# Optimization experiments

Measured on AMD Instinct MI355X. Metric: run time of the kernel, lower is better.

## Reference

```python
import jax, jax.numpy as jnp
import numpy as np

N = 4096      # batch (e.g. nodes)
MUL = 128     # multiplicity of every irrep chunk
INV_SQRT3 = 1.0 / float(np.sqrt(3.0))  # CG norm for 1x1->0 and 0x1->1 / 1x0->1
INV_SQRT6 = 1.0 / float(np.sqrt(6.0))  # CG norm for 1x1->1 (Levi-Civita / sqrt(6))

# Levi-Civita tensor eps[i,j,k]
_EPS = np.zeros((3, 3, 3), dtype=np.float32)
for a, b, c in [(0, 1, 2), (1, 2, 0), (2, 0, 1)]:
    _EPS[a, b, c] = 1.0
    _EPS[a, c, b] = -1.0
EPS = jnp.asarray(_EPS)


def setup_inputs() -> dict:
    key = jax.random.key(0)
    ks = jax.random.split(key, 9)
    # e3nn path normalization folded into weight init std:
    # std = 1/sqrt(mul1*mul2*num_paths_into_that_output_irrep)
    std2 = 1.0 / float(np.sqrt(MUL * MUL * 2))  # scalar out: 2 paths
    std3 = 1.0 / float(np.sqrt(MUL * MUL * 3))  # vector out: 3 paths
    W = (MUL, MUL, MUL)
    return {
        "x1_s": jax.random.normal(ks[0], (N, MUL), dtype=jnp.float32),
        "x1_v": jax.random.normal(ks[1], (N, MUL, 3), dtype=jnp.float32),
        "x2_s": jax.random.normal(ks[2], (N, MUL), dtype=jnp.float32),
        "x2_v": jax.random.normal(ks[3], (N, MUL, 3), dtype=jnp.float32),
        "w_sss": jax.random.normal(ks[4], W, dtype=jnp.float32) * std2,
        "w_vvs": jax.random.normal(ks[5], W, dtype=jnp.float32) * std2,
        "w_svv": jax.random.normal(ks[6], W, dtype=jnp.float32) * std3,
        "w_vsv": jax.random.normal(ks[7], W, dtype=jnp.float32) * std3,
        "w_vvv": jax.random.normal(ks[8], W, dtype=jnp.float32) * std3,
    }


def reference(x1_s, x1_v, x2_s, x2_v, w_sss, w_vvs, w_svv, w_vsv, w_vvv):
    # ---- paths into 0e (scalar) output ----
    # 0e x 0e -> 0e : CG = 1
    a = jnp.einsum('nu,uvw->nvw', x1_s, w_sss)           # [N,MUL,MUL]
    out_s = jnp.einsum('nvw,nv->nw', a, x2_s)            # [N,MUL]
    # 1o x 1o -> 0e : CG = delta_ij / sqrt(3)
    dot = jnp.einsum('nui,nvi->nuv', x1_v, x2_v) * INV_SQRT3
    out_s = out_s + jnp.einsum('nuv,uvw->nw', dot, w_vvs)
    # ---- paths into 1o (vector) output ----
    # 0e x 1o -> 1o : CG = delta / sqrt(3)
    b = jnp.einsum('nu,uvw->nvw', x1_s, w_svv)
    out_v = jnp.einsum('nvw,nvk->nwk', b, x2_v) * INV_SQRT3   # [N,MUL,3]
    # 1o x 0e -> 1o : CG = delta / sqrt(3)
    c = jnp.einsum('nv,uvw->nuw', x2_s, w_vsv)
    out_v = out_v + jnp.einsum('nuw,nuk->nwk', c, x1_v) * INV_SQRT3
    # 1o x 1o -> 1o : CG = eps_ijk / sqrt(6)  (cross product)
    c1 = jnp.einsum('nvj,ijk->nvik', x2_v, EPS)               # [N,MUL,3,3]
    cross = jnp.einsum('nui,nvik->nuvk', x1_v, c1)            # [N,MUL,MUL,3]
    out_v = out_v + jnp.einsum('nuvk,uvw->nwk', cross, w_vvv) * INV_SQRT6
    # pack IrrepsArray 128x0e+128x1o as flat [N, 128 + 384]
    return jnp.concatenate([out_s, out_v.reshape(out_v.shape[0], -1)], axis=-1)
```

## Files before the change

### kernel.cpp

```cpp
#include <hip/hip_runtime.h>
#include <hip/hip_bf16.h>


typedef _Float16 f16;
typedef _Float16 f16x8 __attribute__((ext_vector_type(8)));
typedef float f32x4 __attribute__((ext_vector_type(4)));
typedef unsigned u32;

#define WT_BYTES  (5u*4u*128u*4096u*2u)
#define X1_BYTES  (32u*4u*16384u*2u)
#define SLICE_EL  655360u
#define CHUNK_EL  5120u

__device__ __forceinline__ u32 pkmul16(u32 a, u32 b){
    u32 r; asm("v_pk_mul_f16 %0, %1, %2" : "=v"(r) : "v"(a), "v"(b)); return r;
}
__device__ __forceinline__ u32 pkfma16(u32 a, u32 b, u32 c){
    u32 r; asm("v_pk_fma_f16 %0, %1, %2, %3" : "=v"(r) : "v"(a), "v"(b), "v"(c)); return r;
}
__device__ __forceinline__ u32 pkfma16n(u32 a, u32 b, u32 c){
    u32 r; asm("v_pk_fma_f16 %0, %1, %2, %3 neg_lo:[1,0,0] neg_hi:[1,0,0]"
               : "=v"(r) : "v"(a), "v"(b), "v"(c)); return r;
}

union Frag { u32 u[4]; f16x8 v; };
__device__ __forceinline__ f16x8 FR(const u32 a[4]){
    Frag f; f.u[0]=a[0]; f.u[1]=a[1]; f.u[2]=a[2]; f.u[3]=a[3]; return f.v;
}

__device__ __forceinline__ void gl_lds16(const f16* g, f16* l) {
    __builtin_amdgcn_global_load_lds(
        (const __attribute__((address_space(1))) void*)g,
        (__attribute__((address_space(3))) void*)l,
        16, 0, 0);
}

__global__ __launch_bounds__(256) void pack_w_kernel(
    const float* __restrict__ w0, const float* __restrict__ w1,
    const float* __restrict__ w2, const float* __restrict__ w3,
    const float* __restrict__ w4, f16* __restrict__ wt)
{
    __shared__ float tl[64][130];
    const int b = blockIdx.x;
    const int p = b >> 7;
    const int u = b & 127;
    const int usec = u >> 5;
    const int uin  = u & 31;
    const float* src = (p==0)?w0:(p==1)?w1:(p==2)?w2:(p==3)?w3:w4;
    const float scale = (p==0)?1.0f:(p==4)?0.40824829046386302f:0.57735026918962576f;

    for (int h = 0; h < 2; ++h) {
        const float* spR = src + (size_t)u*16384 + (size_t)h*8192;
        #pragma unroll
        for (int k = 0; k < 8; ++k) {
            const int e4 = (k*256 + threadIdx.x) * 4;
            const float4 v4 = *(const float4*)(spR + e4);
            const int vi = e4 >> 7, w = e4 & 127;
            tl[vi][w+0]=v4.x; tl[vi][w+1]=v4.y; tl[vi][w+2]=v4.z; tl[vi][w+3]=v4.w;
        }
        __syncthreads();
        #pragma unroll
        for (int k = 0; k < 4; ++k) {
            const int cid = k*256 + threadIdx.x;
            const int vbh  = cid >> 9;
            const int wsec = (cid >> 7) & 3;
            const int w    = (cid >> 2) & 31;
            const int q    = cid & 3;
            const int vb   = h*2 + vbh;
            const int c    = vb*32 + uin;
            const int qs   = q ^ ((w >> 1) & 3);
            f16x8 t8;
            #pragma unroll
            for (int j = 0; j < 8; ++j)
                t8[j] = (f16)(tl[vbh*32 + q*8 + j][wsec*32 + w] * scale);
            *(f16x8*)(wt + (size_t)(usec*4 + wsec)*SLICE_EL + (size_t)c*CHUNK_EL
                          + p*1024 + w*32 + qs*8) = t8;
        }
        __syncthreads();
    }
}

__global__ __launch_bounds__(256) void pack_x_kernel(
    const float* __restrict__ x1s, const float* __restrict__ x1v,
    const float* __restrict__ x2s, const float* __restrict__ x2v,
    f16* __restrict__ x1g, f16* __restrict__ x2g)
{
    if (blockIdx.x < 128) {
        __shared__ uint2 tl[128][33];
        const int nb = blockIdx.x;
        #pragma unroll
        for (int k = 0; k < 16; ++k) {
            const int idx = k*256 + threadIdx.x;
            const int u = idx & 127, nd = idx >> 7;
            const size_t i = (size_t)(nb*32 + nd)*128 + u;
            union { f16 h[4]; uint2 u2; } tp;
            tp.h[0] = (f16)x1s[i];
            tp.h[1] = (f16)x1v[i*3 + 0];
            tp.h[2] = (f16)x1v[i*3 + 1];
            tp.h[3] = (f16)x1v[i*3 + 2];
            tl[u][nd] = tp.u2;
        }
        __syncthreads();
        uint2* og = (uint2*)x1g;
        const int t = nb >> 2, nd0 = (nb & 3) * 32;
        #pragma unroll
        for (int k = 0; k < 16; ++k) {
            const int idx = k*256 + threadIdx.x;
            const int u = idx >> 5, nd = idx & 31;
            og[(((t*4 + (u>>5))*32 + (u&31)) << 7) + nd0 + nd] = tl[u][nd];
        }
    } else {
        const int tt = (blockIdx.x - 128)*256 + threadIdx.x;
        const int n = tt >> 7, v = tt & 127;
        const size_t b = (size_t)n*512;
        const size_t i = (size_t)n*128 + v;
        x2g[b +   0 + v] = (f16)x2s[i];
        x2g[b + 128 + v] = (f16)x2v[i*3 + 0];
        x2g[b + 256 + v] = (f16)x2v[i*3 + 1];
        x2g[b + 384 + v] = (f16)x2v[i*3 + 2];
    }
}

__global__ __launch_bounds__(512, 4) void tp_main(
    const f16* __restrict__ wt, const f16* __restrict__ x1g,
    const f16* __restrict__ x2g, float* __restrict__ out)
{
    __shared__ __align__(16) f16 wlds[4*CHUNK_EL];
    __shared__ __align__(16) f16 x1lds[16384];

    const int tid  = threadIdx.x;
    const int lane = tid & 63;
    const int wv   = tid >> 6;
    const int kg   = lane >> 4;
    const int lr   = lane & 15;

    const int b    = blockIdx.x;
    const int s    = (b & 7)*2 + ((b >> 3) & 1);
    const int t    = b >> 4;
    const int usec = s >> 2;
    const int wsec = s & 3;

    const f16* wstream = wt + (size_t)s * SLICE_EL;

    int boff[2];
    #pragma unroll
    for (int ct = 0; ct < 2; ++ct) {
        const int wp = ct*16 + lr;
        boff[ct] = wp*32 + ((kg ^ ((wp >> 1) & 3)) * 8);
    }

    {
        const f16* src = x1g + ((size_t)(t*4 + usec) << 14);
        #pragma unroll
        for (int r = 0; r < 4; ++r)
            gl_lds16(src + (wv*4 + r)*512 + lane*8, x1lds + (wv*4 + r)*512);
    }
    if (wv < 5) {
        #pragma unroll
        for (int k = 0; k < 2; ++k) {
            const f16* sc = wstream + k*CHUNK_EL + wv*1024 + lane*8;
            f16* dc = wlds + k*CHUNK_EL + wv*1024;
            gl_lds16(sc, dc);
            gl_lds16(sc + 512, dc + 512);
        }
    }
    __syncthreads();

    f32x4 acc[2][4];
    #pragma unroll
    for (int c2 = 0; c2 < 2; ++c2)
        #pragma unroll
        for (int d = 0; d < 4; ++d)
            acc[c2][d] = (f32x4){0.f, 0.f, 0.f, 0.f};

    u32 xq[4][4];
    const f16* wsrc = wstream + 2*CHUNK_EL + wv*1024 + lane*8;
    const f16* x2base = x2g + ((size_t)(t*128 + wv*16 + lr) << 9) + kg*8;

    for (int vb = 0; vb < 4; ++vb) {
        {
            const f16* xb = x2base + vb*32;
            #pragma unroll
            for (int q = 0; q < 4; ++q) {
                const uint4 h = *(const uint4*)(xb + (q << 7));
                xq[q][0] = h.x; xq[q][1] = h.y; xq[q][2] = h.z; xq[q][3] = h.w;
            }
        }
        for (int u2b = 0; u2b < 32; u2b += 4) {
            #pragma unroll
            for (int uu = 0; uu < 4; ++uu) {
                const int u2 = u2b + uu;
                const int c  = vb*32 + u2;

                if (c < 126 && wv < 5) {
                    f16* dc = wlds + ((uu + 2) & 3)*CHUNK_EL + wv*1024;
                    gl_lds16(wsrc, dc);
                    gl_lds16(wsrc + 512, dc + 512);
                }
                wsrc += CHUNK_EL;

                if (c < 126)       { asm volatile("s_waitcnt vmcnt(4)" ::: "memory"); }
                else if (c == 126) { asm volatile("s_waitcnt vmcnt(2)" ::: "memory"); }
                else               { asm volatile("s_waitcnt vmcnt(0)" ::: "memory"); }
                __builtin_amdgcn_s_barrier();
                __builtin_amdgcn_sched_barrier(0);

                f16x8 bfr[5][2];
                const f16* wb = wlds + uu*CHUNK_EL;
                #pragma unroll
                for (int p = 0; p < 5; ++p)
                    #pragma unroll
                    for (int ct = 0; ct < 2; ++ct)
                        bfr[p][ct] = *(const f16x8*)(wb + p*1024 + boff[ct]);

                const uint2 h1 = *(const uint2*)(x1lds + u2*512 + (wv*16 + lr)*4);
                const u32 ps1 = __builtin_amdgcn_perm(h1.x, h1.x, 0x01000100u);
                u32 pv[3];
                pv[0] = __builtin_amdgcn_perm(h1.x, h1.x, 0x03020302u);
                pv[1] = __builtin_amdgcn_perm(h1.y, h1.y, 0x01000100u);
                pv[2] = __builtin_amdgcn_perm(h1.y, h1.y, 0x03020302u);

                {
                    u32 f0[4], f1[4];
                    #pragma unroll
                    for (int j = 0; j < 4; ++j) {
                        f0[j] = pkmul16(ps1, xq[0][j]);
                        u32 d = pkmul16(pv[0], xq[1][j]);
                        d     = pkfma16(pv[1], xq[2][j], d);
                        f1[j] = pkfma16(pv[2], xq[3][j], d);
                    }
                    #pragma unroll
                    for (int ct = 0; ct < 2; ++ct) {
                        acc[ct][0] = __builtin_amdgcn_mfma_f32_16x16x32_f16(FR(f0), bfr[0][ct], acc[ct][0], 0,0,0);
                        acc[ct][0] = __builtin_amdgcn_mfma_f32_16x16x32_f16(FR(f1), bfr[1][ct], acc[ct][0], 0,0,0);
                    }
                }
                #pragma unroll
                for (int k = 0; k < 3; ++k) {
                    const int k1 = (k+1) % 3, k2 = (k+2) % 3;
                    u32 fa[4], fb[4], fc[4];
                    #pragma unroll
                    for (int j = 0; j < 4; ++j) {
                        fa[j] = pkmul16(ps1,    xq[1+k][j]);
                        fb[j] = pkmul16(pv[k],  xq[0][j]);
                        u32 tx = pkmul16(pv[k1], xq[1+k2][j]);
                        fc[j] = pkfma16n(pv[k2], xq[1+k1][j], tx);
                    }
                    #pragma unroll
                    for (int ct = 0; ct < 2; ++ct) {
                        acc[ct][1+k] = __builtin_amdgcn_mfma_f32_16x16x32_f16(FR(fa), bfr[2][ct], acc[ct][1+k], 0,0,0);
                        acc[ct][1+k] = __builtin_amdgcn_mfma_f32_16x16x32_f16(FR(fb), bfr[3][ct], acc[ct][1+k], 0,0,0);
                        acc[ct][1+k] = __builtin_amdgcn_mfma_f32_16x16x32_f16(FR(fc), bfr[4][ct], acc[ct][1+k], 0,0,0);
                    }
                }
            }
        }
    }

    #pragma unroll
    for (int ct = 0; ct < 2; ++ct) {
        const int w = wsec*32 + ct*16 + lr;
        #pragma unroll
        for (int j = 0; j < 4; ++j) {
            const int n = t*128 + wv*16 + kg*4 + j;
            float* op = out + (size_t)n*512;
            unsafeAtomicAdd(op + w,             acc[ct][0][j]);
            unsafeAtomicAdd(op + 128 + w*3 + 0, acc[ct][1][j]);
            unsafeAtomicAdd(op + 128 + w*3 + 1, acc[ct][2][j]);
            unsafeAtomicAdd(op + 128 + w*3 + 2, acc[ct][3][j]);
        }
    }
}

extern "C" void kernel_launch(void* const* d_in, const int* in_sizes, int n_in,
                              void* d_out, int out_size, void* d_ws, size_t ws_size,
                              hipStream_t stream)
{
    const float* x1s = (const float*)d_in[0];
    const float* x1v = (const float*)d_in[1];
    const float* x2s = (const float*)d_in[2];
    const float* x2v = (const float*)d_in[3];
    const float* w0  = (const float*)d_in[4];
    const float* w1  = (const float*)d_in[5];
    const float* w2  = (const float*)d_in[6];
    const float* w3  = (const float*)d_in[7];
    const float* w4  = (const float*)d_in[8];

    f16* wtb = (f16*)d_ws;
    f16* x1g = (f16*)((char*)d_ws + WT_BYTES);
    f16* x2g = (f16*)((char*)d_ws + WT_BYTES + X1_BYTES);
    float* out = (float*)d_out;

    pack_w_kernel<<<640, 256, 0, stream>>>(w0, w1, w2, w3, w4, wtb);
    pack_x_kernel<<<2176, 256, 0, stream>>>(x1s, x1v, x2s, x2v, x1g, x2g);
    hipMemsetAsync(d_out, 0, (size_t)out_size*sizeof(float), stream);
    tp_main<<<512, 512, 0, stream>>>(wtb, x1g, x2g, out);
}
```

Before: 239.5 us.

## Halve block size, give each wave two row tiles to reuse weight fragments

```diff
diff --git a/kernel.cpp b/kernel.cpp
--- a/kernel.cpp
+++ b/kernel.cpp
@@ -4,6 +4,7 @@
 
 typedef _Float16 f16;
 typedef _Float16 f16x8 __attribute__((ext_vector_type(8)));
+typedef _Float16 h2 __attribute__((ext_vector_type(2)));
 typedef float f32x4 __attribute__((ext_vector_type(4)));
 typedef unsigned u32;
 
@@ -12,21 +13,9 @@
 #define SLICE_EL  655360u
 #define CHUNK_EL  5120u
 
-__device__ __forceinline__ u32 pkmul16(u32 a, u32 b){
-    u32 r; asm("v_pk_mul_f16 %0, %1, %2" : "=v"(r) : "v"(a), "v"(b)); return r;
-}
-__device__ __forceinline__ u32 pkfma16(u32 a, u32 b, u32 c){
-    u32 r; asm("v_pk_fma_f16 %0, %1, %2, %3" : "=v"(r) : "v"(a), "v"(b), "v"(c)); return r;
-}
-__device__ __forceinline__ u32 pkfma16n(u32 a, u32 b, u32 c){
-    u32 r; asm("v_pk_fma_f16 %0, %1, %2, %3 neg_lo:[1,0,0] neg_hi:[1,0,0]"
-               : "=v"(r) : "v"(a), "v"(b), "v"(c)); return r;
-}
-
-union Frag { u32 u[4]; f16x8 v; };
-__device__ __forceinline__ f16x8 FR(const u32 a[4]){
-    Frag f; f.u[0]=a[0]; f.u[1]=a[1]; f.u[2]=a[2]; f.u[3]=a[3]; return f.v;
-}
+__device__ __forceinline__ h2 bc(u32 x){ union{u32 u; h2 h;} c; c.u=x; return c.h; }
+
+union F8 { h2 h[4]; f16x8 v; };
 
 __device__ __forceinline__ void gl_lds16(const f16* g, f16* l) {
     __builtin_amdgcn_global_load_lds(
@@ -121,7 +110,7 @@
     }
 }
 
-__global__ __launch_bounds__(512, 4) void tp_main(
+__global__ __launch_bounds__(256, 2) void tp_main(
     const f16* __restrict__ wt, const f16* __restrict__ x1g,
     const f16* __restrict__ x2g, float* __restrict__ out)
 {
@@ -152,38 +141,41 @@
     {
         const f16* src = x1g + ((size_t)(t*4 + usec) << 14);
         #pragma unroll
-        for (int r = 0; r < 4; ++r)
-            gl_lds16(src + (wv*4 + r)*512 + lane*8, x1lds + (wv*4 + r)*512);
-    }
-    if (wv < 5) {
-        #pragma unroll
-        for (int k = 0; k < 2; ++k) {
-            const f16* sc = wstream + k*CHUNK_EL + wv*1024 + lane*8;
-            f16* dc = wlds + k*CHUNK_EL + wv*1024;
-            gl_lds16(sc, dc);
-            gl_lds16(sc + 512, dc + 512);
-        }
+        for (int r = 0; r < 8; ++r)
+            gl_lds16(src + r*2048 + tid*8, x1lds + r*2048 + wv*512 + lane*8);
+    }
+    #pragma unroll
+    for (int k = 0; k < 2; ++k) {
+        const f16* sc = wstream + k*CHUNK_EL + wv*1280 + lane*8;
+        f16* dc = wlds + k*CHUNK_EL + wv*1280;
+        gl_lds16(sc, dc);
+        gl_lds16(sc + 512, dc + 512);
+        if (lane < 32) gl_lds16(sc + 1024, dc + 1024);
     }
     __syncthreads();
 
-    f32x4 acc[2][4];
-    #pragma unroll
-    for (int c2 = 0; c2 < 2; ++c2)
-        #pragma unroll
-        for (int d = 0; d < 4; ++d)
-            acc[c2][d] = (f32x4){0.f, 0.f, 0.f, 0.f};
-
-    u32 xq[4][4];
-    const f16* wsrc = wstream + 2*CHUNK_EL + wv*1024 + lane*8;
-    const f16* x2base = x2g + ((size_t)(t*128 + wv*16 + lr) << 9) + kg*8;
+    f32x4 acc[2][2][4];
+    #pragma unroll
+    for (int rt = 0; rt < 2; ++rt)
+        #pragma unroll
+        for (int c2 = 0; c2 < 2; ++c2)
+            #pragma unroll
+            for (int d = 0; d < 4; ++d)
+                acc[rt][c2][d] = (f32x4){0.f, 0.f, 0.f, 0.f};
+
+    h2 xq[2][4][4];
+    const f16* wsrc = wstream + 2*CHUNK_EL + wv*1280 + lane*8;
 
     for (int vb = 0; vb < 4; ++vb) {
-        {
-            const f16* xb = x2base + vb*32;
+        #pragma unroll
+        for (int rt = 0; rt < 2; ++rt) {
+            const int n = t*128 + wv*32 + rt*16 + lr;
+            const f16* xb = x2g + ((size_t)n << 9) + kg*8 + vb*32;
             #pragma unroll
             for (int q = 0; q < 4; ++q) {
                 const uint4 h = *(const uint4*)(xb + (q << 7));
-                xq[q][0] = h.x; xq[q][1] = h.y; xq[q][2] = h.z; xq[q][3] = h.w;
+                xq[rt][q][0] = bc(h.x); xq[rt][q][1] = bc(h.y);
+                xq[rt][q][2] = bc(h.z); xq[rt][q][3] = bc(h.w);
             }
         }
         for (int u2b = 0; u2b < 32; u2b += 4) {
@@ -192,16 +184,17 @@
                 const int u2 = u2b + uu;
                 const int c  = vb*32 + u2;
 
-                if (c < 126 && wv < 5) {
-                    f16* dc = wlds + ((uu + 2) & 3)*CHUNK_EL + wv*1024;
+                if (c < 126) {
+                    f16* dc = wlds + ((uu + 2) & 3)*CHUNK_EL + wv*1280;
                     gl_lds16(wsrc, dc);
                     gl_lds16(wsrc + 512, dc + 512);
+                    if (lane < 32) gl_lds16(wsrc + 1024, dc + 1024);
                 }
                 wsrc += CHUNK_EL;
 
-                if (c < 126)       { asm volatile("s_waitcnt vmcnt(4)" ::: "memory"); }
-                else if (c == 126) { asm volatile("s_waitcnt vmcnt(2)" ::: "memory"); }
-                else               { asm volatile("s_waitcnt vmcnt(0)" ::: "memory"); }
+                if (u2 == 0 || c == 126) { asm volatile("s_waitcnt vmcnt(3)" ::: "memory"); }
+                else if (c == 127)       { asm volatile("s_waitcnt vmcnt(0)" ::: "memory"); }
+                else                     { asm volatile("s_waitcnt vmcnt(6)" ::: "memory"); }
                 __builtin_amdgcn_s_barrier();
                 __builtin_amdgcn_sched_barrier(0);
 
@@ -213,44 +206,47 @@
                     for (int ct = 0; ct < 2; ++ct)
                         bfr[p][ct] = *(const f16x8*)(wb + p*1024 + boff[ct]);
 
-                const uint2 h1 = *(const uint2*)(x1lds + u2*512 + (wv*16 + lr)*4);
-                const u32 ps1 = __builtin_amdgcn_perm(h1.x, h1.x, 0x01000100u);
-                u32 pv[3];
-                pv[0] = __builtin_amdgcn_perm(h1.x, h1.x, 0x03020302u);
-                pv[1] = __builtin_amdgcn_perm(h1.y, h1.y, 0x01000100u);
-                pv[2] = __builtin_amdgcn_perm(h1.y, h1.y, 0x03020302u);
-
-                {
-                    u32 f0[4], f1[4];
-                    #pragma unroll
-                    for (int j = 0; j < 4; ++j) {
-                        f0[j] = pkmul16(ps1, xq[0][j]);
-                        u32 d = pkmul16(pv[0], xq[1][j]);
-                        d     = pkfma16(pv[1], xq[2][j], d);
-                        f1[j] = pkfma16(pv[2], xq[3][j], d);
+                #pragma unroll
+                for (int rt = 0; rt < 2; ++rt) {
+                    const uint2 h1 = *(const uint2*)(x1lds + u2*512 + (wv*32 + rt*16 + lr)*4);
+                    const h2 ps1 = bc(__builtin_amdgcn_perm(h1.x, h1.x, 0x01000100u));
+                    h2 pv[3];
+                    pv[0] = bc(__builtin_amdgcn_perm(h1.x, h1.x, 0x03020302u));
+                    pv[1] = bc(__builtin_amdgcn_perm(h1.y, h1.y, 0x01000100u));
+                    pv[2] = bc(__builtin_amdgcn_perm(h1.y, h1.y, 0x03020302u));
+
+                    {
+                        F8 f0, f1;
+                        #pragma unroll
+                        for (int j = 0; j < 4; ++j) {
+                            f0.h[j] = ps1 * xq[rt][0][j];
+                            h2 d = pv[0] * xq[rt][1][j];
+                            d = __builtin_elementwise_fma(pv[1], xq[rt][2][j], d);
+                            f1.h[j] = __builtin_elementwise_fma(pv[2], xq[rt][3][j], d);
+                        }
+                        #pragma unroll
+                        for (int ct = 0; ct < 2; ++ct) {
+                            acc[rt][ct][0] = __builtin_amdgcn_mfma_f32_16x16x32_f16(f0.v, bfr[0][ct], acc[rt][ct][0], 0,0,0);
+                            acc[rt][ct][0] = __builtin_amdgcn_mfma_f32_16x16x32_f16(f1.v, bfr[1][ct], acc[rt][ct][0], 0,0,0);
+                        }
                     }
                     #pragma unroll
-                    for (int ct = 0; ct < 2; ++ct) {
-                        acc[ct][0] = __builtin_amdgcn_mfma_f32_16x16x32_f16(FR(f0), bfr[0][ct], acc[ct][0], 0,0,0);
-                        acc[ct][0] = __builtin_amdgcn_mfma_f32_16x16x32_f16(FR(f1), bfr[1][ct], acc[ct][0], 0,0,0);
-                    }
-                }
-                #pragma unroll
-                for (int k = 0; k < 3; ++k) {
-                    const int k1 = (k+1) % 3, k2 = (k+2) % 3;
-                    u32 fa[4], fb[4], fc[4];
-                    #pragma unroll
-                    for (int j = 0; j < 4; ++j) {
-                        fa[j] = pkmul16(ps1,    xq[1+k][j]);
-                        fb[j] = pkmul16(pv[k],  xq[0][j]);
-                        u32 tx = pkmul16(pv[k1], xq[1+k2][j]);
-                        fc[j] = pkfma16n(pv[k2], xq[1+k1][j], tx);
-                    }
-                    #pragma unroll
-                    for (int ct = 0; ct < 2; ++ct) {
-                        acc[ct][1+k] = __builtin_amdgcn_mfma_f32_16x16x32_f16(FR(fa), bfr[2][ct], acc[ct][1+k], 0,0,0);
-                        acc[ct][1+k] = __builtin_amdgcn_mfma_f32_16x16x32_f16(FR(fb), bfr[3][ct], acc[ct][1+k], 0,0,0);
-                        acc[ct][1+k] = __builtin_amdgcn_mfma_f32_16x16x32_f16(FR(fc), bfr[4][ct], acc[ct][1+k], 0,0,0);
+                    for (int k = 0; k < 3; ++k) {
+                        const int k1 = (k+1) % 3, k2 = (k+2) % 3;
+                        F8 fa, fb, fc;
+                        #pragma unroll
+                        for (int j = 0; j < 4; ++j) {
+                            fa.h[j] = ps1   * xq[rt][1+k][j];
+                            fb.h[j] = pv[k] * xq[rt][0][j];
+                            h2 tx = pv[k1] * xq[rt][1+k2][j];
+                            fc.h[j] = __builtin_elementwise_fma(-pv[k2], xq[rt][1+k1][j], tx);
+                        }
+                        #pragma unroll
+                        for (int ct = 0; ct < 2; ++ct) {
+                            acc[rt][ct][1+k] = __builtin_amdgcn_mfma_f32_16x16x32_f16(fa.v, bfr[2][ct], acc[rt][ct][1+k], 0,0,0);
+                            acc[rt][ct][1+k] = __builtin_amdgcn_mfma_f32_16x16x32_f16(fb.v, bfr[3][ct], acc[rt][ct][1+k], 0,0,0);
+                            acc[rt][ct][1+k] = __builtin_amdgcn_mfma_f32_16x16x32_f16(fc.v, bfr[4][ct], acc[rt][ct][1+k], 0,0,0);
+                        }
                     }
                 }
             }
@@ -258,16 +254,19 @@
     }
 
     #pragma unroll
-    for (int ct = 0; ct < 2; ++ct) {
-        const int w = wsec*32 + ct*16 + lr;
-        #pragma unroll
-        for (int j = 0; j < 4; ++j) {
-            const int n = t*128 + wv*16 + kg*4 + j;
-            float* op = out + (size_t)n*512;
-            unsafeAtomicAdd(op + w,             acc[ct][0][j]);
-            unsafeAtomicAdd(op + 128 + w*3 + 0, acc[ct][1][j]);
-            unsafeAtomicAdd(op + 128 + w*3 + 1, acc[ct][2][j]);
-            unsafeAtomicAdd(op + 128 + w*3 + 2, acc[ct][3][j]);
+    for (int rt = 0; rt < 2; ++rt) {
+        #pragma unroll
+        for (int ct = 0; ct < 2; ++ct) {
+            const int w = wsec*32 + ct*16 + lr;
+            #pragma unroll
+            for (int j = 0; j < 4; ++j) {
+                const int n = t*128 + wv*32 + rt*16 + kg*4 + j;
+                float* op = out + (size_t)n*512;
+                unsafeAtomicAdd(op + w,             acc[rt][ct][0][j]);
+                unsafeAtomicAdd(op + 128 + w*3 + 0, acc[rt][ct][1][j]);
+                unsafeAtomicAdd(op + 128 + w*3 + 1, acc[rt][ct][2][j]);
+                unsafeAtomicAdd(op + 128 + w*3 + 2, acc[rt][ct][3][j]);
+            }
         }
     }
 }
@@ -294,5 +293,5 @@
     pack_w_kernel<<<640, 256, 0, stream>>>(w0, w1, w2, w3, w4, wtb);
     pack_x_kernel<<<2176, 256, 0, stream>>>(x1s, x1v, x2s, x2v, x1g, x2g);
     hipMemsetAsync(d_out, 0, (size_t)out_size*sizeof(float), stream);
-    tp_main<<<512, 512, 0, stream>>>(wtb, x1g, x2g, out);
-}
+    tp_main<<<512, 256, 0, stream>>>(wtb, x1g, x2g, out);
+}
```

Result: no change. 239.7 us (+0.1%).
